# Performance work log

Measured on AMD Instinct MI355X. Metric: run time of the kernel, lower is better.

The kernel has to match this reference:

```python
import jax, jax.numpy as jnp
import numpy as np

N_HEAD = 16


def setup_inputs() -> dict:
    key = jax.random.key(0)
    ks = jax.random.split(key, 5)
    B, T, C = 4, 2048, 1024
    s = 0.02
    x = jax.random.normal(ks[0], (B, T, C), jnp.float32)
    wq = jax.random.normal(ks[1], (C, C), jnp.float32) * s
    wk = jax.random.normal(ks[2], (C, C), jnp.float32) * s
    wv = jax.random.normal(ks[3], (C, C), jnp.float32) * s
    wp = jax.random.normal(ks[4], (C, C), jnp.float32) * s
    zb = jnp.zeros((C,), jnp.float32)
    return {"x": x, "wq": wq, "bq": zb, "wk": wk, "bk": zb,
            "wv": wv, "bv": zb, "wp": wp, "bp": zb}


def _rope_cos_sin(T, D):
    half = D // 2
    i = jnp.arange(half, dtype=jnp.float32)
    alpha = 1.0 / (10000.0 ** (2.0 * i / D))        # [half]
    ang = jnp.arange(T, dtype=jnp.float32)[:, None] * alpha  # [T, half]
    return jnp.cos(ang), jnp.sin(ang)


def _apply_rope(t, cos, sin):
    # t: [B, H, T, D]; non-interleaved halves as in the torch module
    half = t.shape[-1] // 2
    xr, xi = t[..., :half], t[..., half:]
    return jnp.concatenate([xr * cos - xi * sin, xr * sin + xi * cos], axis=-1)


def reference(x, wq, bq, wk, bk, wv, bv, wp, bp):
    B, T, C = x.shape
    H = N_HEAD
    D = C // H
    # QKV projections (torch Linear: x @ W.T + b)
    def heads(w, b):
        return (x @ w.T + b).reshape(B, T, H, D).transpose(0, 2, 1, 3)
    q, k, v = heads(wq, bq), heads(wk, bk), heads(wv, bv)
    cos, sin = _rope_cos_sin(T, D)  # each [T, D//2], broadcasts over B,H
    q = _apply_rope(q, cos, sin)
    k = _apply_rope(k, cos, sin)
    scale = 1.0 / np.sqrt(D).astype(np.float32)
    att = jnp.einsum('bhtd,bhsd->bhts', q, k) * scale  # [B,H,T,T]
    causal = jnp.tril(jnp.ones((T, T), bool))
    att = jnp.where(causal, att, jnp.float32(-jnp.inf))
    att = jax.nn.softmax(att, axis=-1)
    y = jnp.einsum('bhts,bhsd->bhtd', att, v)  # [B,H,T,D]
    y = y.transpose(0, 2, 1, 3).reshape(B, T, C)
    return y @ wp.T + bp
```

## Files before the change

kernel.cpp:

```cpp
#include <hip/hip_runtime.h>
#include <math.h>

constexpr int B = 4, T = 2048, C = 1024, H = 16, D = 64;
constexpr int M = B * T;
constexpr size_t BTC = (size_t)B * T * C;
constexpr float QSCALE = 0.18033688011112042f;
constexpr float ROPE_C = -0.415241011861f;

typedef short bf16x8 __attribute__((ext_vector_type(8)));
typedef float f32x4 __attribute__((ext_vector_type(4)));

__device__ inline ushort f2bf(float f) {
  union { float f; unsigned u; } cv; cv.f = f;
  unsigned u = cv.u;
  u += 0x7fffu + ((u >> 16) & 1u);
  return (ushort)(u >> 16);
}
__device__ inline ushort f2bfr(float f) {
  union { float f; unsigned u; } cv; cv.f = f;
  return (ushort)((cv.u + 0x8000u) >> 16);
}

__device__ inline void async_load16(const void* g, void* l) {
  __builtin_amdgcn_global_load_lds(
      (const __attribute__((address_space(1))) void*)g,
      (__attribute__((address_space(3))) void*)l, 16, 0, 0);
}

__device__ __forceinline__ bf16x8 ones_frag() {
  bf16x8 v;
#pragma unroll
  for (int i = 0; i < 8; i++) v[i] = (short)0x3F80;
  return v;
}

__global__ __launch_bounds__(256) void f32_to_bf16(
    const float* __restrict__ in, ushort* __restrict__ outp) {
  int i = (blockIdx.x * 256 + threadIdx.x) * 4;
  float4 v = *(const float4*)(in + i);
  ushort4 o;
  o.x = f2bf(v.x); o.y = f2bf(v.y); o.z = f2bf(v.z); o.w = f2bf(v.w);
  *(ushort4*)(outp + i) = o;
}

__global__ __launch_bounds__(256) void conv_weights(
    const float* __restrict__ w0, const float* __restrict__ w1,
    const float* __restrict__ w2, const float* __restrict__ w3,
    ushort* __restrict__ outp) {
  const int seg_blocks = (C * C) / 1024;
  int seg = blockIdx.x / seg_blocks;
  int blk = blockIdx.x - seg * seg_blocks;
  const float* src = (seg == 0) ? w0 : (seg == 1) ? w1 : (seg == 2) ? w2 : w3;
  int i = (blk * 256 + threadIdx.x) * 4;
  float4 v = *(const float4*)(src + i);
  ushort4 o;
  o.x = f2bf(v.x); o.y = f2bf(v.y); o.z = f2bf(v.z); o.w = f2bf(v.w);
  *(ushort4*)(outp + (size_t)seg * C * C + i) = o;
}

constexpr int QNT = C / 64;

template <int OM, int NCT>
__global__ __launch_bounds__(512, 2) void gemm_pipe(
    const ushort* __restrict__ A, const ushort* __restrict__ Wt,
    const float* __restrict__ b0, const float* __restrict__ b1,
    const float* __restrict__ b2, void* __restrict__ out1,
    void* __restrict__ out2, void* __restrict__ out3) {
  __shared__ ushort As[2][256 * 64] __attribute__((aligned(16)));
  __shared__ ushort Bs[3][128 * 64] __attribute__((aligned(16)));
  const int tid = threadIdx.x;
  const int lane = tid & 63;
  const int lrow = lane & 15, quad = lane >> 4;
  const int wave = tid >> 6;
  const int wr = wave >> 1, wc = wave & 1;
  const int x7 = lrow & 7;

  int bid = blockIdx.y * NCT + blockIdx.x;
  const int cpx = NCT * 4;
  int lin = (bid & 7) * cpx + (bid >> 3);
  int row0 = (lin / NCT) * 256;
  int col0 = (lin % NCT) * 128;

  unsigned gaA[4], gaB[2];
#pragma unroll
  for (int i = 0; i < 4; i++) {
    int c = tid + i * 512;
    int r = c >> 3, cl = c & 7;
    gaA[i] = (unsigned)(row0 + r) * C + (cl ^ (r & 7)) * 8;
  }
#pragma unroll
  for (int i = 0; i < 2; i++) {
    int c = tid + i * 512;
    int r = c >> 3, cl = c & 7;
    gaB[i] = (unsigned)(col0 + r) * C + (cl ^ (r & 7)) * 8;
  }

  f32x4 acc[4][4];
#pragma unroll
  for (int i = 0; i < 4; i++)
#pragma unroll
    for (int j = 0; j < 4; j++) acc[i][j] = (f32x4){0.f, 0.f, 0.f, 0.f};

#pragma unroll
  for (int i = 0; i < 4; i++)
    async_load16(A + gaA[i], &As[0][(tid + i * 512) * 8]);
#pragma unroll
  for (int i = 0; i < 2; i++)
    async_load16(Wt + gaB[i], &Bs[0][(tid + i * 512) * 8]);
#pragma unroll
  for (int i = 0; i < 2; i++)
    async_load16(Wt + gaB[i] + 64, &Bs[1][(tid + i * 512) * 8]);
  asm volatile("s_waitcnt vmcnt(2)" ::: "memory");
  __builtin_amdgcn_sched_barrier(0);
  __builtin_amdgcn_s_barrier();

  int bi = 0;
  for (int t = 0; t < QNT; ++t) {
    const int pa = t & 1;
    const ushort* Ap = As[pa];
    const ushort* Bp = Bs[bi];
    int bi2 = bi - 1; if (bi2 < 0) bi2 = 2;

    {
      const int slot = (quad ^ x7) * 8;
      bf16x8 aF[4], bF[4];
#pragma unroll
      for (int i = 0; i < 4; i++)
        aF[i] = *(const bf16x8*)&Ap[(wr * 64 + i * 16 + lrow) * 64 + slot];
#pragma unroll
      for (int j = 0; j < 4; j++)
        bF[j] = *(const bf16x8*)&Bp[(wc * 64 + j * 16 + lrow) * 64 + slot];
      if (t + 1 < QNT) {
#pragma unroll
        for (int i = 0; i < 4; i++)
          async_load16(A + gaA[i] + (t + 1) * 64,
                       &As[pa ^ 1][(tid + i * 512) * 8]);
      }
      __builtin_amdgcn_s_setprio(1);
#pragma unroll
      for (int i = 0; i < 4; i++)
#pragma unroll
        for (int j = 0; j < 4; j++)
          acc[i][j] = __builtin_amdgcn_mfma_f32_16x16x32_bf16(
              aF[i], bF[j], acc[i][j], 0, 0, 0);
      __builtin_amdgcn_s_setprio(0);
    }

    {
      const int slot = ((4 + quad) ^ x7) * 8;
      bf16x8 aF[4], bF[4];
#pragma unroll
      for (int i = 0; i < 4; i++)
        aF[i] = *(const bf16x8*)&Ap[(wr * 64 + i * 16 + lrow) * 64 + slot];
#pragma unroll
      for (int j = 0; j < 4; j++)
        bF[j] = *(const bf16x8*)&Bp[(wc * 64 + j * 16 + lrow) * 64 + slot];
      if (t + 2 < QNT) {
#pragma unroll
        for (int i = 0; i < 2; i++)
          async_load16(Wt + gaB[i] + (t + 2) * 64,
                       &Bs[bi2][(tid + i * 512) * 8]);
      }
      __builtin_amdgcn_s_setprio(1);
#pragma unroll
      for (int i = 0; i < 4; i++)
#pragma unroll
        for (int j = 0; j < 4; j++)
          acc[i][j] = __builtin_amdgcn_mfma_f32_16x16x32_bf16(
              aF[i], bF[j], acc[i][j], 0, 0, 0);
      __builtin_amdgcn_s_setprio(0);
    }

    if (t + 2 < QNT) {
      asm volatile("s_waitcnt vmcnt(2)" ::: "memory");
    } else {
      asm volatile("s_waitcnt vmcnt(0)" ::: "memory");
    }
    __builtin_amdgcn_sched_barrier(0);
    __builtin_amdgcn_s_barrier();
    bi = (bi == 2) ? 0 : bi + 1;
  }

  const int nb = col0 + wc * 64;
  const int mbase = row0 + wr * 64;
  const float* bias = (col0 < 1024) ? b0 : (col0 < 2048) ? b1 : b2;
  float bn[4];
#pragma unroll
  for (int j = 0; j < 4; j++) bn[j] = bias[(nb & 1023) + j * 16 + lrow];

  if (OM == 0) {
    const int N = NCT * 128;
    float* outp = (float*)out1;
#pragma unroll
    for (int i = 0; i < 4; i++)
#pragma unroll
      for (int j = 0; j < 4; j++) {
        int n = nb + j * 16 + lrow;
#pragma unroll
        for (int r = 0; r < 4; r++) {
          int m = mbase + i * 16 + quad * 4 + r;
          outp[(size_t)m * N + n] = acc[i][j][r] + bn[j];
        }
      }
  } else {
    int seg = nb >> 10;
    int hh = (nb & 1023) >> 6;
    if (seg < 2) {
      ushort* dst = (seg == 0) ? (ushort*)out1 : (ushort*)out2;
      float scale = (seg == 0) ? QSCALE : 1.0f;
      float a0 = __builtin_amdgcn_exp2f((float)lrow * ROPE_C);
      float a1 = __builtin_amdgcn_exp2f((float)(lrow + 16) * ROPE_C);
#pragma unroll
      for (int i = 0; i < 4; i++) {
#pragma unroll
        for (int r = 0; r < 4; r++) {
          int m = mbase + i * 16 + quad * 4 + r;
          int tt = m & (T - 1), bb = m >> 11;
          float s0, c0, s1, c1;
          __sincosf((float)tt * a0, &s0, &c0);
          __sincosf((float)tt * a1, &s1, &c1);
          float xr0 = acc[i][0][r] + bn[0];
          float xi0 = acc[i][2][r] + bn[2];
          float xr1 = acc[i][1][r] + bn[1];
          float xi1 = acc[i][3][r] + bn[3];
          ushort* pp = dst + ((size_t)(bb * H + hh) * T + tt) * D + lrow;
          pp[0]  = f2bf((xr0 * c0 - xi0 * s0) * scale);
          pp[32] = f2bf((xr0 * s0 + xi0 * c0) * scale);
          pp[16] = f2bf((xr1 * c1 - xi1 * s1) * scale);
          pp[48] = f2bf((xr1 * s1 + xi1 * c1) * scale);
        }
      }
    } else {
      ushort* dst = (ushort*)out3;
#pragma unroll
      for (int i = 0; i < 4; i++) {
        int m0 = mbase + i * 16 + quad * 4;
        int t0 = m0 & (T - 1), bb = m0 >> 11;
        size_t base = (size_t)(bb * H + hh) * D * T + t0;
#pragma unroll
        for (int j = 0; j < 4; j++) {
          int d = j * 16 + lrow;
          ushort4 pk;
          pk.x = f2bf(acc[i][j][0] + bn[j]);
          pk.y = f2bf(acc[i][j][1] + bn[j]);
          pk.z = f2bf(acc[i][j][2] + bn[j]);
          pk.w = f2bf(acc[i][j][3] + bn[j]);
          *(ushort4*)(dst + base + (size_t)d * T) = pk;
        }
      }
    }
  }
}

__device__ __forceinline__ void stage_kv(
    const ushort* kbh, const ushort* vbh, int s0,
    ushort* Kl, ushort* Vl, int tid) {
#pragma unroll
  for (int i = 0; i < 2; i++) {
    int c = tid + i * 256;
    int r = c >> 3, cc = c & 7;
    int g = (cc ^ (r & 7)) * 8;
    async_load16(kbh + (size_t)(s0 + r) * D + g, Kl + c * 8);
    async_load16(vbh + (size_t)r * T + s0 + g, Vl + c * 8);
  }
}

template <int MODE>
__device__ __forceinline__ void attn_step4(
    int s0, const ushort* KL, const ushort* VL, ushort* P,
    const bf16x8 (&qf)[2][2], int lrow, int quad, int sw0, int sw1,
    int qg0, int qg1, f32x4 (&o)[4][2], f32x4 (&ol)[2]) {
  bf16x8 kf0[4], kf1[4];
#pragma unroll
  for (int kt = 0; kt < 4; kt++) {
    int base = (kt * 16 + lrow) * 64;
    kf0[kt] = *(const bf16x8*)&KL[base + sw0];
    kf1[kt] = *(const bf16x8*)&KL[base + sw1];
  }
  bf16x8 vf0[4], vf1[4];
#pragma unroll
  for (int ds = 0; ds < 4; ds++) {
    int base = (ds * 16 + lrow) * 64;
    vf0[ds] = *(const bf16x8*)&VL[base + sw0];
    vf1[ds] = *(const bf16x8*)&VL[base + sw1];
  }
#pragma unroll
  for (int g = 0; g < 2; g++) {
    if (MODE == 2 && g == 0) continue;
    int qg = g ? qg1 : qg0;
    f32x4 st[4];
#pragma unroll
    for (int kt = 0; kt < 4; kt++) {
      f32x4 z = {0.f, 0.f, 0.f, 0.f};
      st[kt] = __builtin_amdgcn_mfma_f32_16x16x32_bf16(kf0[kt], qf[g][0], z, 0, 0, 0);
      st[kt] = __builtin_amdgcn_mfma_f32_16x16x32_bf16(kf1[kt], qf[g][1], st[kt], 0, 0, 0);
    }
    if ((MODE == 1 && g == 0) || (MODE == 2 && g == 1)) {
#pragma unroll
      for (int kt = 0; kt < 4; kt++)
#pragma unroll
        for (int r = 0; r < 4; r++)
          if (s0 + kt * 16 + quad * 4 + r > qg) st[kt][r] = -1e30f;
    }
#pragma unroll
    for (int kt = 0; kt < 4; kt++) {
      ushort4 pk;
      pk.x = f2bfr(__builtin_amdgcn_exp2f(st[kt][0]));
      pk.y = f2bfr(__builtin_amdgcn_exp2f(st[kt][1]));
      pk.z = f2bfr(__builtin_amdgcn_exp2f(st[kt][2]));
      pk.w = f2bfr(__builtin_amdgcn_exp2f(st[kt][3]));
      *(ushort4*)&P[((2 * kt + (quad >> 1)) * 32 + g * 16 + lrow) * 8 + (quad & 1) * 4] = pk;
    }
  }
  asm volatile("" ::: "memory");
  bf16x8 ones = ones_frag();
#pragma unroll
  for (int g = 0; g < 2; g++) {
    if (MODE == 2 && g == 0) continue;
    bf16x8 pf0 = *(const bf16x8*)&P[(quad * 32 + g * 16 + lrow) * 8];
    bf16x8 pf1 = *(const bf16x8*)&P[((quad + 4) * 32 + g * 16 + lrow) * 8];
    ol[g] = __builtin_amdgcn_mfma_f32_16x16x32_bf16(ones, pf0, ol[g], 0, 0, 0);
    ol[g] = __builtin_amdgcn_mfma_f32_16x16x32_bf16(ones, pf1, ol[g], 0, 0, 0);
#pragma unroll
    for (int ds = 0; ds < 4; ds++) {
      o[ds][g] = __builtin_amdgcn_mfma_f32_16x16x32_bf16(vf0[ds], pf0, o[ds][g], 0, 0, 0);
      o[ds][g] = __builtin_amdgcn_mfma_f32_16x16x32_bf16(vf1[ds], pf1, o[ds][g], 0, 0, 0);
    }
  }
}

__global__ __launch_bounds__(256, 3) void attn_mfma4(
    const ushort* __restrict__ qb_, const ushort* __restrict__ kb_,
    const ushort* __restrict__ vtb_, ushort* __restrict__ y) {
  __shared__ ushort Kl[2][64 * 64] __attribute__((aligned(16)));
  __shared__ ushort Vl[2][64 * 64] __attribute__((aligned(16)));
  __shared__ ushort Pl[4][2048] __attribute__((aligned(16)));
  int tid = threadIdx.x;
  int wave = tid >> 6, lane = tid & 63;
  int lrow = lane & 15, quad = lane >> 4;
  int qbi = 15 - (int)(blockIdx.x >> 6);
  int bh = blockIdx.x & 63;
  int b = bh >> 4, h = bh & 15;
  int Q0 = qbi * 128;
  ushort* P = Pl[wave];
  const ushort* kbh = kb_ + (size_t)bh * T * D;
  const ushort* vbh = vtb_ + (size_t)bh * D * T;

  int qg0 = Q0 + wave * 16 + lrow;
  int qg1 = qg0 + 64;
  bf16x8 qf[2][2];
  {
    const ushort* qp0 = qb_ + ((size_t)bh * T + qg0) * D + quad * 8;
    qf[0][0] = *(const bf16x8*)qp0;
    qf[0][1] = *(const bf16x8*)(qp0 + 32);
    const ushort* qp1 = qb_ + ((size_t)bh * T + qg1) * D + quad * 8;
    qf[1][0] = *(const bf16x8*)qp1;
    qf[1][1] = *(const bf16x8*)(qp1 + 32);
  }
  int r7 = lrow & 7;
  int sw0 = (quad ^ r7) * 8;
  int sw1 = ((quad + 4) ^ r7) * 8;

  f32x4 o[4][2];
#pragma unroll
  for (int ds = 0; ds < 4; ds++)
#pragma unroll
    for (int g = 0; g < 2; g++) o[ds][g] = (f32x4){0.f, 0.f, 0.f, 0.f};
  f32x4 ol[2] = {(f32x4){0.f, 0.f, 0.f, 0.f}, (f32x4){0.f, 0.f, 0.f, 0.f}};

  int trips = 2 * qbi + 2;
  stage_kv(kbh, vbh, 0, Kl[0], Vl[0], tid);
  int it = 0;
  for (; it < trips - 2; ++it) {
    __syncthreads();
    stage_kv(kbh, vbh, (it + 1) * 64, Kl[(it + 1) & 1], Vl[(it + 1) & 1], tid);
    attn_step4<0>(it * 64, Kl[it & 1], Vl[it & 1], P, qf, lrow, quad, sw0, sw1,
                  qg0, qg1, o, ol);
  }
  __syncthreads();
  stage_kv(kbh, vbh, (it + 1) * 64, Kl[(it + 1) & 1], Vl[(it + 1) & 1], tid);
  attn_step4<1>(it * 64, Kl[it & 1], Vl[it & 1], P, qf, lrow, quad, sw0, sw1,
                qg0, qg1, o, ol);
  ++it;
  __syncthreads();
  attn_step4<2>(it * 64, Kl[it & 1], Vl[it & 1], P, qf, lrow, quad, sw0, sw1,
                qg0, qg1, o, ol);

#pragma unroll
  for (int g = 0; g < 2; g++) {
    float inv = 1.f / ol[g][0];
    int qg = g ? qg1 : qg0;
#pragma unroll
    for (int ds = 0; ds < 4; ds++) {
      ushort4 pk;
      pk.x = f2bf(o[ds][g][0] * inv);
      pk.y = f2bf(o[ds][g][1] * inv);
      pk.z = f2bf(o[ds][g][2] * inv);
      pk.w = f2bf(o[ds][g][3] * inv);
      *(ushort4*)(y + ((size_t)b * T + qg) * C + h * D + ds * 16 + quad * 4) = pk;
    }
  }
}

extern "C" void kernel_launch(void* const* d_in, const int* in_sizes, int n_in,
                              void* d_out, int out_size, void* d_ws, size_t ws_size,
                              hipStream_t stream) {
  const float* x  = (const float*)d_in[0];
  const float* wq = (const float*)d_in[1];
  const float* bq = (const float*)d_in[2];
  const float* wk = (const float*)d_in[3];
  const float* bk = (const float*)d_in[4];
  const float* wv = (const float*)d_in[5];
  const float* bv = (const float*)d_in[6];
  const float* wp = (const float*)d_in[7];
  const float* bp = (const float*)d_in[8];
  float* out = (float*)d_out;

  ushort* xb    = (ushort*)d_ws;
  ushort* qb    = xb + BTC;
  ushort* kb    = qb + BTC;
  ushort* vtb   = kb + BTC;
  ushort* yb    = vtb + BTC;
  ushort* wqkvb = yb + BTC;
  ushort* wpb   = wqkvb + (size_t)3 * C * C;

  f32_to_bf16<<<(int)(BTC / 1024), 256, 0, stream>>>(x, xb);
  conv_weights<<<4 * (C * C) / 1024, 256, 0, stream>>>(wq, wk, wv, wp, wqkvb);

  dim3 qkv_grid(3 * C / 128, M / 256);
  gemm_pipe<1, 24><<<qkv_grid, 512, 0, stream>>>(
      xb, wqkvb, bq, bk, bv, qb, kb, vtb);

  attn_mfma4<<<(B * H * T / 128), 256, 0, stream>>>(qb, kb, vtb, yb);

  dim3 proj_grid(C / 128, M / 256);
  gemm_pipe<0, 8><<<proj_grid, 512, 0, stream>>>(
      yb, wpb, bp, bp, bp, out, nullptr, nullptr);
}
```

Before: 231.5 us.

## Shrink GEMM tiles to 128x128 with 256 threads and fuse conversion kernels

The projection GEMMs move from a 256x128 tile with 8 waves to a 128x128 tile with 4 waves. That doubles the number of workgroups, which improves CU coverage, particularly for the smaller output projection. The cost is lower reuse of each B tile, and the load counts and vmcnt waits are adjusted to match. The x and weight fp32-to-bf16 conversion kernels are also merged into a single launch to save one launch.

```diff
diff --git a/kernel.cpp b/kernel.cpp
--- a/kernel.cpp
+++ b/kernel.cpp
@@ -34,39 +34,42 @@
   return v;
 }
 
-__global__ __launch_bounds__(256) void f32_to_bf16(
-    const float* __restrict__ in, ushort* __restrict__ outp) {
-  int i = (blockIdx.x * 256 + threadIdx.x) * 4;
-  float4 v = *(const float4*)(in + i);
-  ushort4 o;
-  o.x = f2bf(v.x); o.y = f2bf(v.y); o.z = f2bf(v.z); o.w = f2bf(v.w);
-  *(ushort4*)(outp + i) = o;
-}
-
-__global__ __launch_bounds__(256) void conv_weights(
-    const float* __restrict__ w0, const float* __restrict__ w1,
-    const float* __restrict__ w2, const float* __restrict__ w3,
-    ushort* __restrict__ outp) {
-  const int seg_blocks = (C * C) / 1024;
-  int seg = blockIdx.x / seg_blocks;
-  int blk = blockIdx.x - seg * seg_blocks;
-  const float* src = (seg == 0) ? w0 : (seg == 1) ? w1 : (seg == 2) ? w2 : w3;
-  int i = (blk * 256 + threadIdx.x) * 4;
+__global__ __launch_bounds__(256) void conv_all(
+    const float* __restrict__ x, const float* __restrict__ w0,
+    const float* __restrict__ w1, const float* __restrict__ w2,
+    const float* __restrict__ w3, ushort* __restrict__ xb,
+    ushort* __restrict__ wb) {
+  const int XBLK = (int)(BTC / 1024);
+  const int WBLK = (C * C) / 1024;
+  int blk = blockIdx.x;
+  const float* src;
+  ushort* dst;
+  int i;
+  if (blk < XBLK) {
+    src = x; dst = xb;
+    i = (blk * 256 + threadIdx.x) * 4;
+  } else {
+    int wseg = (blk - XBLK) >> 10;
+    int wblk = (blk - XBLK) & (WBLK - 1);
+    src = (wseg == 0) ? w0 : (wseg == 1) ? w1 : (wseg == 2) ? w2 : w3;
+    dst = wb + (size_t)wseg * C * C;
+    i = (wblk * 256 + threadIdx.x) * 4;
+  }
   float4 v = *(const float4*)(src + i);
   ushort4 o;
   o.x = f2bf(v.x); o.y = f2bf(v.y); o.z = f2bf(v.z); o.w = f2bf(v.w);
-  *(ushort4*)(outp + (size_t)seg * C * C + i) = o;
+  *(ushort4*)(dst + i) = o;
 }
 
 constexpr int QNT = C / 64;
 
 template <int OM, int NCT>
-__global__ __launch_bounds__(512, 2) void gemm_pipe(
+__global__ __launch_bounds__(256, 2) void gemm_pipe(
     const ushort* __restrict__ A, const ushort* __restrict__ Wt,
     const float* __restrict__ b0, const float* __restrict__ b1,
     const float* __restrict__ b2, void* __restrict__ out1,
     void* __restrict__ out2, void* __restrict__ out3) {
-  __shared__ ushort As[2][256 * 64] __attribute__((aligned(16)));
+  __shared__ ushort As[2][128 * 64] __attribute__((aligned(16)));
   __shared__ ushort Bs[3][128 * 64] __attribute__((aligned(16)));
   const int tid = threadIdx.x;
   const int lane = tid & 63;
@@ -76,23 +79,19 @@
   const int x7 = lrow & 7;
 
   int bid = blockIdx.y * NCT + blockIdx.x;
-  const int cpx = NCT * 4;
+  const int cpx = NCT * 8;
   int lin = (bid & 7) * cpx + (bid >> 3);
-  int row0 = (lin / NCT) * 256;
+  int row0 = (lin / NCT) * 128;
   int col0 = (lin % NCT) * 128;
 
-  unsigned gaA[4], gaB[2];
+  unsigned gaA[4], gaB[4];
 #pragma unroll
   for (int i = 0; i < 4; i++) {
-    int c = tid + i * 512;
+    int c = tid + i * 256;
     int r = c >> 3, cl = c & 7;
-    gaA[i] = (unsigned)(row0 + r) * C + (cl ^ (r & 7)) * 8;
-  }
-#pragma unroll
-  for (int i = 0; i < 2; i++) {
-    int c = tid + i * 512;
-    int r = c >> 3, cl = c & 7;
-    gaB[i] = (unsigned)(col0 + r) * C + (cl ^ (r & 7)) * 8;
+    int g = (cl ^ (r & 7)) * 8;
+    gaA[i] = (unsigned)(row0 + r) * C + g;
+    gaB[i] = (unsigned)(col0 + r) * C + g;
   }
 
   f32x4 acc[4][4];
@@ -103,14 +102,14 @@
 
 #pragma unroll
   for (int i = 0; i < 4; i++)
-    async_load16(A + gaA[i], &As[0][(tid + i * 512) * 8]);
-#pragma unroll
-  for (int i = 0; i < 2; i++)
-    async_load16(Wt + gaB[i], &Bs[0][(tid + i * 512) * 8]);
-#pragma unroll
-  for (int i = 0; i < 2; i++)
-    async_load16(Wt + gaB[i] + 64, &Bs[1][(tid + i * 512) * 8]);
-  asm volatile("s_waitcnt vmcnt(2)" ::: "memory");
+    async_load16(A + gaA[i], &As[0][(tid + i * 256) * 8]);
+#pragma unroll
+  for (int i = 0; i < 4; i++)
+    async_load16(Wt + gaB[i], &Bs[0][(tid + i * 256) * 8]);
+#pragma unroll
+  for (int i = 0; i < 4; i++)
+    async_load16(Wt + gaB[i] + 64, &Bs[1][(tid + i * 256) * 8]);
+  asm volatile("s_waitcnt vmcnt(4)" ::: "memory");
   __builtin_amdgcn_sched_barrier(0);
   __builtin_amdgcn_s_barrier();
 
@@ -134,7 +133,7 @@
 #pragma unroll
         for (int i = 0; i < 4; i++)
           async_load16(A + gaA[i] + (t + 1) * 64,
-                       &As[pa ^ 1][(tid + i * 512) * 8]);
+                       &As[pa ^ 1][(tid + i * 256) * 8]);
       }
       __builtin_amdgcn_s_setprio(1);
 #pragma unroll
@@ -157,9 +156,9 @@
         bF[j] = *(const bf16x8*)&Bp[(wc * 64 + j * 16 + lrow) * 64 + slot];
       if (t + 2 < QNT) {
 #pragma unroll
-        for (int i = 0; i < 2; i++)
+        for (int i = 0; i < 4; i++)
           async_load16(Wt + gaB[i] + (t + 2) * 64,
-                       &Bs[bi2][(tid + i * 512) * 8]);
+                       &Bs[bi2][(tid + i * 256) * 8]);
       }
       __builtin_amdgcn_s_setprio(1);
 #pragma unroll
@@ -172,7 +171,7 @@
     }
 
     if (t + 2 < QNT) {
-      asm volatile("s_waitcnt vmcnt(2)" ::: "memory");
+      asm volatile("s_waitcnt vmcnt(4)" ::: "memory");
     } else {
       asm volatile("s_waitcnt vmcnt(0)" ::: "memory");
     }
@@ -189,7 +188,7 @@
   for (int j = 0; j < 4; j++) bn[j] = bias[(nb & 1023) + j * 16 + lrow];
 
   if (OM == 0) {
-    const int N = NCT * 128;
+    const int N = C;
     float* outp = (float*)out1;
 #pragma unroll
     for (int i = 0; i < 4; i++)
@@ -424,16 +423,16 @@
   ushort* wqkvb = yb + BTC;
   ushort* wpb   = wqkvb + (size_t)3 * C * C;
 
-  f32_to_bf16<<<(int)(BTC / 1024), 256, 0, stream>>>(x, xb);
-  conv_weights<<<4 * (C * C) / 1024, 256, 0, stream>>>(wq, wk, wv, wp, wqkvb);
-
-  dim3 qkv_grid(3 * C / 128, M / 256);
-  gemm_pipe<1, 24><<<qkv_grid, 512, 0, stream>>>(
+  conv_all<<<(int)(BTC / 1024) + 4 * (C * C) / 1024, 256, 0, stream>>>(
+      x, wq, wk, wv, wp, xb, wqkvb);
+
+  dim3 qkv_grid(3 * C / 128, M / 128);
+  gemm_pipe<1, 24><<<qkv_grid, 256, 0, stream>>>(
       xb, wqkvb, bq, bk, bv, qb, kb, vtb);
 
   attn_mfma4<<<(B * H * T / 128), 256, 0, stream>>>(qb, kb, vtb, yb);
 
-  dim3 proj_grid(C / 128, M / 256);
-  gemm_pipe<0, 8><<<proj_grid, 512, 0, stream>>>(
+  dim3 proj_grid(C / 128, M / 128);
+  gemm_pipe<0, 8><<<proj_grid, 256, 0, stream>>>(
       yb, wpb, bp, bp, bp, out, nullptr, nullptr);
 }
```

After: 236.3 us. 1.02x slower.
